# Kernel optimization log

Measured on AMD Instinct MI355X. Metric: run time of the kernel, lower is better.

The kernel has to match this reference:

```python
import jax, jax.numpy as jnp
import numpy as np

N = 100_000      # n_nodes
DEG = 32         # edge_threshold (fixed out-degree)
D = 64           # in_channels = out_channels, heads = 1
NEG_SLOPE = 0.2


def setup_inputs() -> dict:
    key = jax.random.key(0)
    k1, k2, k3, k4 = jax.random.split(key, 4)
    x = jax.random.normal(k1, (N, D), jnp.float32)
    # fixed-degree edge list with no self loops (offset in [1, N-1])
    src = jnp.repeat(jnp.arange(N, dtype=jnp.int64), DEG)
    off = jax.random.randint(k2, (N * DEG,), 1, N, dtype=jnp.int64)
    dst = (src + off) % N
    edge_index = jnp.stack([src, dst])  # [2, E]
    # glorot init as in the torch module
    stdv_w = float(np.sqrt(6.0 / (D + D)))
    weight = jax.random.uniform(k3, (D, D), jnp.float32, -stdv_w, stdv_w)
    stdv_a = float(np.sqrt(6.0 / (1 + 2 * D)))  # att is [1, heads=1, 2*D]
    att = jax.random.uniform(k4, (2 * D,), jnp.float32, -stdv_a, stdv_a)
    bias = jnp.zeros((D,), jnp.float32)
    return {"x": x, "edge_index": edge_index, "weight": weight, "att": att, "bias": bias}


def reference(x, edge_index, weight, att, bias):
    n, d = x.shape
    h = x @ weight                               # [N, D] (heads=1)
    # add self loops (inputs are constructed without self loops)
    loop = jnp.arange(n, dtype=edge_index.dtype)
    src = jnp.concatenate([edge_index[0], loop])  # message sources (x_j)
    dst = jnp.concatenate([edge_index[1], loop])  # aggregation targets (x_i)
    # GAT edge score: (cat([x_i, x_j]) * att).sum(-1) = h_i@a_i + h_j@a_j
    a_i, a_j = att[:d], att[d:]
    s_i = h @ a_i                                 # [N]
    s_j = h @ a_j                                 # [N]
    alpha = s_i[dst] + s_j[src]                   # [E+N]
    alpha = jnp.where(alpha > 0, alpha, NEG_SLOPE * alpha)  # leaky_relu
    # segment softmax over destination nodes (numerically stable)
    amax = jax.ops.segment_max(alpha, dst, num_segments=n)
    e = jnp.exp(alpha - amax[dst])
    denom = jax.ops.segment_sum(e, dst, num_segments=n)
    w = e / (denom[dst] + 1e-16)                  # [E+N]
    # weighted scatter-add aggregation of source features
    out = jax.ops.segment_sum(h[src] * w[:, None], dst, num_segments=n)  # [N, D]
    out = out + bias                              # head-mean is identity (heads=1)
    # dropout(p=0.5) is identity in eval mode; F.normalize (L2, dim=1, eps=1e-12)
    norm = jnp.linalg.norm(out, axis=1, keepdims=True)
    return out / jnp.maximum(norm, 1e-12)
```

## Files before the change

### kernel.cpp

```cpp
#include <hip/hip_runtime.h>
#include <math.h>

#define NEG_SLOPE 0.2f
#define NBINS_MAX 392
#define CURSOR_PAD 16
#define CHUNK_B 12500
#define CAPL 72
#define STRL 73
#define GRAN 16
#define CAP_SLOTS 12544
#define COLS_CAP 8704
#define CAPN 96
#define STRN 97
#define SENT 0xFFFFFFFFu

__device__ __forceinline__ unsigned pk_bf16x2(float a, float b) {
    unsigned ua = __float_as_uint(a);
    ua = (ua + 0x7FFFu + ((ua >> 16) & 1u)) >> 16;
    unsigned ub = __float_as_uint(b);
    ub = (ub + 0x7FFFu + ((ub >> 16) & 1u)) & 0xFFFF0000u;
    return ua | ub;
}

__global__ __launch_bounds__(256) void k_linear(const float* __restrict__ x,
        const float* __restrict__ W, const float* __restrict__ att,
        uint2* __restrict__ h16, float* __restrict__ si, float* __restrict__ sj,
        int* __restrict__ bin_cursor, int nbins, int n)
{
    int tid = threadIdx.x;
    int g = blockIdx.x * 256 + tid;
    if (g < nbins * CURSOR_PAD) bin_cursor[g] = 0;

    int lane = tid & 63;
    int wv = tid >> 6;
    int q = lane >> 4;
    int f = lane & 15;

    const float4* W4 = (const float4*)W;
    float4 Wr[16];
#pragma unroll
    for (int kb = 0; kb < 16; ++kb)
        Wr[kb] = W4[(16 * q + kb) * 16 + f];

    const float4* att4 = (const float4*)att;
    float4 ai4 = att4[f];
    float4 aj4 = att4[16 + f];
    const float4* x4 = (const float4*)x;

    int row0 = (blockIdx.x * 4 + wv) * 8;
    for (int r = 0; r < 8; ++r) {
        int row = row0 + r;
        if (row >= n) break;
        size_t xb = (size_t)row * 16 + 4 * q;
        float4 xq0 = x4[xb + 0];
        float4 xq1 = x4[xb + 1];
        float4 xq2 = x4[xb + 2];
        float4 xq3 = x4[xb + 3];
        float4 acc = {0.f, 0.f, 0.f, 0.f};
#define LSTEP(xc, kb) { float4 w4 = Wr[kb]; \
        acc.x = fmaf((xc), w4.x, acc.x); acc.y = fmaf((xc), w4.y, acc.y); \
        acc.z = fmaf((xc), w4.z, acc.z); acc.w = fmaf((xc), w4.w, acc.w); }
        LSTEP(xq0.x, 0)  LSTEP(xq0.y, 1)  LSTEP(xq0.z, 2)  LSTEP(xq0.w, 3)
        LSTEP(xq1.x, 4)  LSTEP(xq1.y, 5)  LSTEP(xq1.z, 6)  LSTEP(xq1.w, 7)
        LSTEP(xq2.x, 8)  LSTEP(xq2.y, 9)  LSTEP(xq2.z, 10) LSTEP(xq2.w, 11)
        LSTEP(xq3.x, 12) LSTEP(xq3.y, 13) LSTEP(xq3.z, 14) LSTEP(xq3.w, 15)
#undef LSTEP
        acc.x += __shfl_xor(acc.x, 16); acc.x += __shfl_xor(acc.x, 32);
        acc.y += __shfl_xor(acc.y, 16); acc.y += __shfl_xor(acc.y, 32);
        acc.z += __shfl_xor(acc.z, 16); acc.z += __shfl_xor(acc.z, 32);
        acc.w += __shfl_xor(acc.w, 16); acc.w += __shfl_xor(acc.w, 32);

        if (q == 0) {
            uint2 p;
            p.x = pk_bf16x2(acc.x, acc.y);
            p.y = pk_bf16x2(acc.z, acc.w);
            h16[(size_t)row * 16 + f] = p;
        }

        float p = acc.x * ai4.x + acc.y * ai4.y + acc.z * ai4.z + acc.w * ai4.w;
        float pq = acc.x * aj4.x + acc.y * aj4.y + acc.z * aj4.z + acc.w * aj4.w;
#pragma unroll
        for (int o = 8; o >= 1; o >>= 1) {
            p += __shfl_xor(p, o);
            pq += __shfl_xor(pq, o);
        }
        if (lane == 0) { si[row] = p; sj[row] = pq; }
    }
}

__global__ __launch_bounds__(512) void k_bin(const int* __restrict__ src,
        const int* __restrict__ dst, int E, int nbins,
        int* __restrict__ bin_cursor, unsigned* __restrict__ bin_edges)
{
    __shared__ unsigned bins[NBINS_MAX * STRL];
    __shared__ int cnt[NBINS_MAX];
    __shared__ int gbase[NBINS_MAX];

    int tid = threadIdx.x;
    int base = blockIdx.x * CHUNK_B;
    int cntE = E - base;
    if (cntE > CHUNK_B) cntE = CHUNK_B;
    int c4 = cntE >> 2;

    for (int b = tid; b < nbins; b += 512) cnt[b] = 0;
    __syncthreads();

#define PLACE(dd, ss) { int bb = (dd) >> 8; int c = atomicAdd(&cnt[bb], 1); \
        if (c < CAPL) bins[bb * STRL + c] = ((unsigned)((dd) & 255) << 17) | (unsigned)(ss); }
    {
        const int4* dst4 = (const int4*)(dst + base);
        const int4* src4 = (const int4*)(src + base);
        for (int i = tid; i < c4; i += 512) {
            int4 d4 = dst4[i];
            int4 s4 = src4[i];
            PLACE(d4.x, s4.x) PLACE(d4.y, s4.y) PLACE(d4.z, s4.z) PLACE(d4.w, s4.w)
        }
        for (int i = (c4 << 2) + tid; i < cntE; i += 512) {
            int dd = dst[base + i]; int ss = src[base + i];
            PLACE(dd, ss)
        }
    }
#undef PLACE
    __syncthreads();

    {
        int start = (blockIdx.x * 97) % nbins;
        for (int k = tid; k < nbins; k += 512) {
            int b = k + start;
            if (b >= nbins) b -= nbins;
            int c = cnt[b];
            if (c > CAPL) c = CAPL;
            int slots = (c + GRAN - 1) & ~(GRAN - 1);
            int g = (slots > 0) ? atomicAdd(&bin_cursor[b * CURSOR_PAD], slots) : 0;
            int allow = CAP_SLOTS - g;
            if (allow < 0) allow = 0;
            if (slots > allow) slots = allow;
            if (c > slots) c = slots;
            cnt[b] = c | (slots << 16);
            gbase[b] = b * CAP_SLOTS + g;
        }
    }
    __syncthreads();

    int lane = tid & 63;
    int wv = tid >> 6;
    for (int b = wv; b < nbins; b += 8) {
        int packed = cnt[b];
        int c = packed & 0xFFFF;
        int slots = packed >> 16;
        unsigned* dp = bin_edges + gbase[b];
        const unsigned* sp = bins + b * STRL;
        if (lane < slots)      dp[lane]      = (lane < c)      ? sp[lane]      : SENT;
        if (lane + 64 < slots) dp[lane + 64] = (lane + 64 < c) ? sp[lane + 64] : SENT;
    }
}

__global__ __launch_bounds__(512) void k_csr(const int* __restrict__ bin_cursor,
        const unsigned* __restrict__ bin_edges, unsigned* __restrict__ cols,
        int* __restrict__ row_start, int* __restrict__ deg, int n)
{
    __shared__ unsigned slots[256 * STRN];
    __shared__ int cntv[256];
    __shared__ int offv[256];
    __shared__ int wsum[4];
    int b = blockIdx.x;
    int tid = threadIdx.x;
    int base = b * CAP_SLOTS;
    int cbase = b * COLS_CAP;
    int cntE = bin_cursor[b * CURSOR_PAD];
    if (cntE > CAP_SLOTS) cntE = CAP_SLOTS;
    int c4 = cntE >> 2;

    if (tid < 256) cntv[tid] = 0;
    __syncthreads();

#define PUT(pkv) { unsigned pk = (pkv); if (pk != SENT) { int nl = (int)(pk >> 17); \
        int c = atomicAdd(&cntv[nl], 1); \
        if (c < CAPN) slots[nl * STRN + c] = pk & 0x1FFFFu; } }
    {
        const uint4* be4 = (const uint4*)(bin_edges + base);
        for (int i = tid; i < c4; i += 512) {
            uint4 p = be4[i];
            PUT(p.x) PUT(p.y) PUT(p.z) PUT(p.w)
        }
        for (int i = (c4 << 2) + tid; i < cntE; i += 512)
            PUT(bin_edges[base + i])
    }
#undef PUT
    __syncthreads();

    int lane = tid & 63;
    int wv = tid >> 6;
    int s = 0, v = 0;
    if (tid < 256) {
        s = cntv[tid];
        if (s > CAPN) s = CAPN;
        v = s;
#pragma unroll
        for (int o = 1; o < 64; o <<= 1) {
            int t = __shfl_up(v, o);
            if (lane >= o) v += t;
        }
        if (lane == 63) wsum[wv] = v;
    }
    __syncthreads();
    if (tid < 256) {
        int woff = 0;
        for (int w = 0; w < wv; ++w) woff += wsum[w];
        int ex = v - s + woff;
        int gd = b * 256 + tid;
        if (gd < n) {
            row_start[gd] = cbase + ex;
            deg[gd] = s;
        }
        offv[tid] = ex;
        cntv[tid] = s;
    }
    __syncthreads();

    for (int nl = wv; nl < 256; nl += 8) {
        int c = cntv[nl];
        int ex = offv[nl];
        if (lane < c)      cols[cbase + ex + lane]      = slots[nl * STRN + lane];
        if (lane + 64 < c) cols[cbase + ex + lane + 64] = slots[nl * STRN + lane + 64];
    }
}

__global__ __launch_bounds__(256) void k_agg(const uint2* __restrict__ h16,
        const float* __restrict__ si, const float* __restrict__ sj,
        const int* __restrict__ row_start, const int* __restrict__ deg_arr,
        const unsigned* __restrict__ cols,
        const float* __restrict__ bias, float* __restrict__ out, int n)
{
    __shared__ int2 swArr[4][132];
    int lane = threadIdx.x & 63;
    int wv = threadIdx.x >> 6;
    int d = blockIdx.x * 4 + wv;
    if (d >= n) return;

    int dg = deg_arr[d];
    if (dg > 128) dg = 128;
    int rs = row_start[d];
    float sid = si[d];

    int s0 = 0, s1 = 0;
    float a0 = -1e30f, a1 = -1e30f;
    if (lane < dg) {
        s0 = (int)cols[rs + lane];
        float t = sid + sj[s0];
        a0 = t > 0.f ? t : NEG_SLOPE * t;
    }
    if (lane + 64 < dg) {
        s1 = (int)cols[rs + lane + 64];
        float t = sid + sj[s1];
        a1 = t > 0.f ? t : NEG_SLOPE * t;
    }
    float tself = sid + sj[d];
    float aself = tself > 0.f ? tself : NEG_SLOPE * tself;

    float m = fmaxf(fmaxf(a0, a1), aself);
#pragma unroll
    for (int o = 32; o >= 1; o >>= 1) m = fmaxf(m, __shfl_xor(m, o));

    float e0 = (lane < dg) ? __expf(a0 - m) : 0.f;
    float e1 = (lane + 64 < dg) ? __expf(a1 - m) : 0.f;
    float eself = __expf(aself - m);

    float dsum = e0 + e1;
#pragma unroll
    for (int o = 32; o >= 1; o >>= 1) dsum += __shfl_xor(dsum, o);
    dsum += eself;

    if (lane < dg) swArr[wv][lane] = make_int2(s0, __float_as_int(e0));
    if (lane + 64 < dg) swArr[wv][lane + 64] = make_int2(s1, __float_as_int(e1));
    if (lane == 0) swArr[wv][dg] = make_int2(d, __float_as_int(eself));
    int cntAll = dg + 1;

    int q = lane >> 4;
    int f = lane & 15;
    int fb = f << 3;
    const char* h8 = (const char*)h16;
    float4 acc0 = {0.f, 0.f, 0.f, 0.f};
    float4 acc1 = {0.f, 0.f, 0.f, 0.f};
    float4 acc2 = {0.f, 0.f, 0.f, 0.f};
    float4 acc3 = {0.f, 0.f, 0.f, 0.f};

#define GLOAD(e) (*(const uint2*)(h8 + (((unsigned)(e) << 7) | fb)))
#define UNPK_FMA(hv, wgt, acc) { \
        acc.x = fmaf((wgt), __uint_as_float((hv).x << 16), acc.x); \
        acc.y = fmaf((wgt), __uint_as_float((hv).x & 0xFFFF0000u), acc.y); \
        acc.z = fmaf((wgt), __uint_as_float((hv).y << 16), acc.z); \
        acc.w = fmaf((wgt), __uint_as_float((hv).y & 0xFFFF0000u), acc.w); }

    int j = q;
    for (; j + 12 < cntAll; j += 16) {
        int2 eA = swArr[wv][j];
        int2 eB = swArr[wv][j + 4];
        int2 eC = swArr[wv][j + 8];
        int2 eD = swArr[wv][j + 12];
        uint2 hA = GLOAD(eA.x);
        uint2 hB = GLOAD(eB.x);
        uint2 hC = GLOAD(eC.x);
        uint2 hD = GLOAD(eD.x);
        float wA = __int_as_float(eA.y);
        float wB = __int_as_float(eB.y);
        float wC = __int_as_float(eC.y);
        float wD = __int_as_float(eD.y);
        UNPK_FMA(hA, wA, acc0)
        UNPK_FMA(hB, wB, acc1)
        UNPK_FMA(hC, wC, acc2)
        UNPK_FMA(hD, wD, acc3)
    }
    for (; j + 4 < cntAll; j += 8) {
        int2 eA = swArr[wv][j];
        int2 eB = swArr[wv][j + 4];
        uint2 hA = GLOAD(eA.x);
        uint2 hB = GLOAD(eB.x);
        float wA = __int_as_float(eA.y);
        float wB = __int_as_float(eB.y);
        UNPK_FMA(hA, wA, acc0)
        UNPK_FMA(hB, wB, acc1)
    }
    if (j < cntAll) {
        int2 eA = swArr[wv][j];
        uint2 hA = GLOAD(eA.x);
        float wA = __int_as_float(eA.y);
        UNPK_FMA(hA, wA, acc0)
    }
#undef UNPK_FMA
#undef GLOAD

    acc0.x += acc1.x; acc0.y += acc1.y; acc0.z += acc1.z; acc0.w += acc1.w;
    acc2.x += acc3.x; acc2.y += acc3.y; acc2.z += acc3.z; acc2.w += acc3.w;
    acc0.x += acc2.x; acc0.y += acc2.y; acc0.z += acc2.z; acc0.w += acc2.w;

    acc0.x += __shfl_xor(acc0.x, 16); acc0.x += __shfl_xor(acc0.x, 32);
    acc0.y += __shfl_xor(acc0.y, 16); acc0.y += __shfl_xor(acc0.y, 32);
    acc0.z += __shfl_xor(acc0.z, 16); acc0.z += __shfl_xor(acc0.z, 32);
    acc0.w += __shfl_xor(acc0.w, 16); acc0.w += __shfl_xor(acc0.w, 32);

    float inv = 1.f / (dsum + 1e-16f);
    const float4* b4 = (const float4*)bias;
    float4 bb = b4[f];
    float4 o4;
    o4.x = acc0.x * inv + bb.x;
    o4.y = acc0.y * inv + bb.y;
    o4.z = acc0.z * inv + bb.z;
    o4.w = acc0.w * inv + bb.w;

    float nsq = o4.x * o4.x + o4.y * o4.y + o4.z * o4.z + o4.w * o4.w;
#pragma unroll
    for (int o = 8; o >= 1; o >>= 1) nsq += __shfl_xor(nsq, o);
    float rn = 1.f / fmaxf(sqrtf(nsq), 1e-12f);

    if (q == 0) {
        float4 res;
        res.x = o4.x * rn; res.y = o4.y * rn; res.z = o4.z * rn; res.w = o4.w * rn;
        ((float4*)out)[(size_t)d * 16 + f] = res;
    }
}

extern "C" void kernel_launch(void* const* d_in, const int* in_sizes, int n_in,
                              void* d_out, int out_size, void* d_ws, size_t ws_size,
                              hipStream_t stream)
{
    const float* x    = (const float*)d_in[0];
    const int*   ei   = (const int*)d_in[1];
    const float* W    = (const float*)d_in[2];
    const float* att  = (const float*)d_in[3];
    const float* bias = (const float*)d_in[4];
    float* out = (float*)d_out;

    int n = in_sizes[0] / 64;
    int E = in_sizes[1] / 2;
    const int* src = ei;
    const int* dst = ei + E;

    int nbins = (n + 255) >> 8;
    int NCH = (E + CHUNK_B - 1) / CHUNK_B;

    char* ws = (char*)d_ws;
#define CARVE(ptr, type, count) type* ptr = (type*)ws; \
        ws += (((size_t)(count) * sizeof(type)) + 255) & ~(size_t)255;
    CARVE(h16, uint2, (size_t)n * 16)
    CARVE(si, float, n)
    CARVE(sj, float, n)
    CARVE(row_start, int, n)
    CARVE(deg, int, n)
    CARVE(bin_cursor, int, (size_t)NBINS_MAX * CURSOR_PAD)
    CARVE(bin_edges, unsigned, (size_t)nbins * CAP_SLOTS)
    CARVE(cols, unsigned, (size_t)nbins * COLS_CAP)
#undef CARVE

    k_linear<<<(n + 31) / 32, 256, 0, stream>>>(x, W, att, h16, si, sj, bin_cursor, nbins, n);
    k_bin<<<NCH, 512, 0, stream>>>(src, dst, E, nbins, bin_cursor, bin_edges);
    k_csr<<<nbins, 512, 0, stream>>>(bin_cursor, bin_edges, cols, row_start, deg, n);
    k_agg<<<(n + 3) / 4, 256, 0, stream>>>(h16, si, sj, row_start, deg, cols, bias, out, n);
}
```

Measured before the change: 238.9 us.

## Fuse CSR construction and attention aggregation into one per-bin kernel

Merges k_csr and k_agg into a single kernel. Each 256-node bin's neighbour lists stay in shared memory, and waves loop over that bin's destination nodes to run the softmax and weighted gather there. This removes the global cols/row_start/deg arrays, their write and re-read, and one kernel launch. The trade-off is far fewer blocks: one per bin, with a large shared-memory footprint, so less parallelism is available to hide gather latency. Per-node capacity also drops to 72 in-edges.

```diff
diff --git a/kernel.cpp b/kernel.cpp
--- a/kernel.cpp
+++ b/kernel.cpp
@@ -9,9 +9,8 @@
 #define STRL 73
 #define GRAN 16
 #define CAP_SLOTS 12544
-#define COLS_CAP 8704
-#define CAPN 96
-#define STRN 97
+#define CAPN 72
+#define STRN 73
 #define SENT 0xFFFFFFFFu
 
 __device__ __forceinline__ unsigned pk_bf16x2(float a, float b) {
@@ -155,18 +154,17 @@
     }
 }
 
-__global__ __launch_bounds__(512) void k_csr(const int* __restrict__ bin_cursor,
-        const unsigned* __restrict__ bin_edges, unsigned* __restrict__ cols,
-        int* __restrict__ row_start, int* __restrict__ deg, int n)
+__global__ __launch_bounds__(512) void k_fused(const int* __restrict__ bin_cursor,
+        const unsigned* __restrict__ bin_edges, const uint2* __restrict__ h16,
+        const float* __restrict__ si, const float* __restrict__ sj,
+        const float* __restrict__ bias, float* __restrict__ out, int n)
 {
     __shared__ unsigned slots[256 * STRN];
     __shared__ int cntv[256];
-    __shared__ int offv[256];
-    __shared__ int wsum[4];
+    __shared__ float ew[8][80];
     int b = blockIdx.x;
     int tid = threadIdx.x;
     int base = b * CAP_SLOTS;
-    int cbase = b * COLS_CAP;
     int cntE = bin_cursor[b * CURSOR_PAD];
     if (cntE > CAP_SLOTS) cntE = CAP_SLOTS;
     int c4 = cntE >> 2;
@@ -191,99 +189,58 @@
 
     int lane = tid & 63;
     int wv = tid >> 6;
-    int s = 0, v = 0;
-    if (tid < 256) {
-        s = cntv[tid];
-        if (s > CAPN) s = CAPN;
-        v = s;
-#pragma unroll
-        for (int o = 1; o < 64; o <<= 1) {
-            int t = __shfl_up(v, o);
-            if (lane >= o) v += t;
-        }
-        if (lane == 63) wsum[wv] = v;
-    }
-    __syncthreads();
-    if (tid < 256) {
-        int woff = 0;
-        for (int w = 0; w < wv; ++w) woff += wsum[w];
-        int ex = v - s + woff;
-        int gd = b * 256 + tid;
-        if (gd < n) {
-            row_start[gd] = cbase + ex;
-            deg[gd] = s;
-        }
-        offv[tid] = ex;
-        cntv[tid] = s;
-    }
-    __syncthreads();
-
-    for (int nl = wv; nl < 256; nl += 8) {
-        int c = cntv[nl];
-        int ex = offv[nl];
-        if (lane < c)      cols[cbase + ex + lane]      = slots[nl * STRN + lane];
-        if (lane + 64 < c) cols[cbase + ex + lane + 64] = slots[nl * STRN + lane + 64];
-    }
-}
-
-__global__ __launch_bounds__(256) void k_agg(const uint2* __restrict__ h16,
-        const float* __restrict__ si, const float* __restrict__ sj,
-        const int* __restrict__ row_start, const int* __restrict__ deg_arr,
-        const unsigned* __restrict__ cols,
-        const float* __restrict__ bias, float* __restrict__ out, int n)
-{
-    __shared__ int2 swArr[4][132];
-    int lane = threadIdx.x & 63;
-    int wv = threadIdx.x >> 6;
-    int d = blockIdx.x * 4 + wv;
-    if (d >= n) return;
-
-    int dg = deg_arr[d];
-    if (dg > 128) dg = 128;
-    int rs = row_start[d];
-    float sid = si[d];
-
-    int s0 = 0, s1 = 0;
-    float a0 = -1e30f, a1 = -1e30f;
-    if (lane < dg) {
-        s0 = (int)cols[rs + lane];
-        float t = sid + sj[s0];
-        a0 = t > 0.f ? t : NEG_SLOPE * t;
-    }
-    if (lane + 64 < dg) {
-        s1 = (int)cols[rs + lane + 64];
-        float t = sid + sj[s1];
-        a1 = t > 0.f ? t : NEG_SLOPE * t;
-    }
-    float tself = sid + sj[d];
-    float aself = tself > 0.f ? tself : NEG_SLOPE * tself;
-
-    float m = fmaxf(fmaxf(a0, a1), aself);
-#pragma unroll
-    for (int o = 32; o >= 1; o >>= 1) m = fmaxf(m, __shfl_xor(m, o));
-
-    float e0 = (lane < dg) ? __expf(a0 - m) : 0.f;
-    float e1 = (lane + 64 < dg) ? __expf(a1 - m) : 0.f;
-    float eself = __expf(aself - m);
-
-    float dsum = e0 + e1;
-#pragma unroll
-    for (int o = 32; o >= 1; o >>= 1) dsum += __shfl_xor(dsum, o);
-    dsum += eself;
-
-    if (lane < dg) swArr[wv][lane] = make_int2(s0, __float_as_int(e0));
-    if (lane + 64 < dg) swArr[wv][lane + 64] = make_int2(s1, __float_as_int(e1));
-    if (lane == 0) swArr[wv][dg] = make_int2(d, __float_as_int(eself));
-    int cntAll = dg + 1;
-
     int q = lane >> 4;
     int f = lane & 15;
     int fb = f << 3;
     const char* h8 = (const char*)h16;
-    float4 acc0 = {0.f, 0.f, 0.f, 0.f};
-    float4 acc1 = {0.f, 0.f, 0.f, 0.f};
-    float4 acc2 = {0.f, 0.f, 0.f, 0.f};
-    float4 acc3 = {0.f, 0.f, 0.f, 0.f};
+    const float4* b4p = (const float4*)bias;
+    float4 bb = b4p[f];
+
+    for (int nl = wv; nl < 256; nl += 8) {
+        int d = b * 256 + nl;
+        if (d >= n) break;
+        int dg = cntv[nl];
+        if (dg > CAPN) dg = CAPN;
+        float sid = si[d];
+        unsigned* scol = slots + nl * STRN;
+
+        int s0 = 0, s1 = 0;
+        float a0 = -1e30f, a1 = -1e30f;
+        if (lane < dg) {
+            s0 = (int)scol[lane];
+            float t = sid + sj[s0];
+            a0 = t > 0.f ? t : NEG_SLOPE * t;
+        }
+        if (lane + 64 < dg) {
+            s1 = (int)scol[lane + 64];
+            float t = sid + sj[s1];
+            a1 = t > 0.f ? t : NEG_SLOPE * t;
+        }
+        float tself = sid + sj[d];
+        float aself = tself > 0.f ? tself : NEG_SLOPE * tself;
+
+        float m = fmaxf(fmaxf(a0, a1), aself);
+#pragma unroll
+        for (int o = 32; o >= 1; o >>= 1) m = fmaxf(m, __shfl_xor(m, o));
+
+        float e0 = (lane < dg) ? __expf(a0 - m) : 0.f;
+        float e1 = (lane + 64 < dg) ? __expf(a1 - m) : 0.f;
+        float eself = __expf(aself - m);
+
+        float dsum = e0 + e1;
+#pragma unroll
+        for (int o = 32; o >= 1; o >>= 1) dsum += __shfl_xor(dsum, o);
+        dsum += eself;
+
+        if (lane < dg) ew[wv][lane] = e0;
+        if (lane + 64 < dg) ew[wv][lane + 64] = e1;
+        if (lane == 0) { scol[dg] = (unsigned)d; ew[wv][dg] = eself; }
+        int cntAll = dg + 1;
+
+        float4 acc0 = {0.f, 0.f, 0.f, 0.f};
+        float4 acc1 = {0.f, 0.f, 0.f, 0.f};
+        float4 acc2 = {0.f, 0.f, 0.f, 0.f};
+        float4 acc3 = {0.f, 0.f, 0.f, 0.f};
 
 #define GLOAD(e) (*(const uint2*)(h8 + (((unsigned)(e) << 7) | fb)))
 #define UNPK_FMA(hv, wgt, acc) { \
@@ -292,71 +249,63 @@
         acc.z = fmaf((wgt), __uint_as_float((hv).y << 16), acc.z); \
         acc.w = fmaf((wgt), __uint_as_float((hv).y & 0xFFFF0000u), acc.w); }
 
-    int j = q;
-    for (; j + 12 < cntAll; j += 16) {
-        int2 eA = swArr[wv][j];
-        int2 eB = swArr[wv][j + 4];
-        int2 eC = swArr[wv][j + 8];
-        int2 eD = swArr[wv][j + 12];
-        uint2 hA = GLOAD(eA.x);
-        uint2 hB = GLOAD(eB.x);
-        uint2 hC = GLOAD(eC.x);
-        uint2 hD = GLOAD(eD.x);
-        float wA = __int_as_float(eA.y);
-        float wB = __int_as_float(eB.y);
-        float wC = __int_as_float(eC.y);
-        float wD = __int_as_float(eD.y);
-        UNPK_FMA(hA, wA, acc0)
-        UNPK_FMA(hB, wB, acc1)
-        UNPK_FMA(hC, wC, acc2)
-        UNPK_FMA(hD, wD, acc3)
-    }
-    for (; j + 4 < cntAll; j += 8) {
-        int2 eA = swArr[wv][j];
-        int2 eB = swArr[wv][j + 4];
-        uint2 hA = GLOAD(eA.x);
-        uint2 hB = GLOAD(eB.x);
-        float wA = __int_as_float(eA.y);
-        float wB = __int_as_float(eB.y);
-        UNPK_FMA(hA, wA, acc0)
-        UNPK_FMA(hB, wB, acc1)
-    }
-    if (j < cntAll) {
-        int2 eA = swArr[wv][j];
-        uint2 hA = GLOAD(eA.x);
-        float wA = __int_as_float(eA.y);
-        UNPK_FMA(hA, wA, acc0)
-    }
+        int j = q;
+        for (; j + 12 < cntAll; j += 16) {
+            unsigned sA = scol[j];      float wA = ew[wv][j];
+            unsigned sB = scol[j + 4];  float wB = ew[wv][j + 4];
+            unsigned sC = scol[j + 8];  float wC = ew[wv][j + 8];
+            unsigned sD = scol[j + 12]; float wD = ew[wv][j + 12];
+            uint2 hA = GLOAD(sA);
+            uint2 hB = GLOAD(sB);
+            uint2 hC = GLOAD(sC);
+            uint2 hD = GLOAD(sD);
+            UNPK_FMA(hA, wA, acc0)
+            UNPK_FMA(hB, wB, acc1)
+            UNPK_FMA(hC, wC, acc2)
+            UNPK_FMA(hD, wD, acc3)
+        }
+        for (; j + 4 < cntAll; j += 8) {
+            unsigned sA = scol[j];     float wA = ew[wv][j];
+            unsigned sB = scol[j + 4]; float wB = ew[wv][j + 4];
+            uint2 hA = GLOAD(sA);
+            uint2 hB = GLOAD(sB);
+            UNPK_FMA(hA, wA, acc0)
+            UNPK_FMA(hB, wB, acc1)
+        }
+        if (j < cntAll) {
+            unsigned sA = scol[j]; float wA = ew[wv][j];
+            uint2 hA = GLOAD(sA);
+            UNPK_FMA(hA, wA, acc0)
+        }
 #undef UNPK_FMA
 #undef GLOAD
 
-    acc0.x += acc1.x; acc0.y += acc1.y; acc0.z += acc1.z; acc0.w += acc1.w;
-    acc2.x += acc3.x; acc2.y += acc3.y; acc2.z += acc3.z; acc2.w += acc3.w;
-    acc0.x += acc2.x; acc0.y += acc2.y; acc0.z += acc2.z; acc0.w += acc2.w;
-
-    acc0.x += __shfl_xor(acc0.x, 16); acc0.x += __shfl_xor(acc0.x, 32);
-    acc0.y += __shfl_xor(acc0.y, 16); acc0.y += __shfl_xor(acc0.y, 32);
-    acc0.z += __shfl_xor(acc0.z, 16); acc0.z += __shfl_xor(acc0.z, 32);
-    acc0.w += __shfl_xor(acc0.w, 16); acc0.w += __shfl_xor(acc0.w, 32);
-
-    float inv = 1.f / (dsum + 1e-16f);
-    const float4* b4 = (const float4*)bias;
-    float4 bb = b4[f];
-    float4 o4;
-    o4.x = acc0.x * inv + bb.x;
-    o4.y = acc0.y * inv + bb.y;
-    o4.z = acc0.z * inv + bb.z;
-    o4.w = acc0.w * inv + bb.w;
-
-    float nsq = o4.x * o4.x + o4.y * o4.y + o4.z * o4.z + o4.w * o4.w;
-#pragma unroll
-    for (int o = 8; o >= 1; o >>= 1) nsq += __shfl_xor(nsq, o);
-    float rn = 1.f / fmaxf(sqrtf(nsq), 1e-12f);
-
-    if (q == 0) {
-        float4 res;
-        res.x = o4.x * rn; res.y = o4.y * rn; res.z = o4.z * rn; res.w = o4.w * rn;
-        ((float4*)out)[(size_t)d * 16 + f] = res;
+        acc0.x += acc1.x; acc0.y += acc1.y; acc0.z += acc1.z; acc0.w += acc1.w;
+        acc2.x += acc3.x; acc2.y += acc3.y; acc2.z += acc3.z; acc2.w += acc3.w;
+        acc0.x += acc2.x; acc0.y += acc2.y; acc0.z += acc2.z; acc0.w += acc2.w;
+
+        acc0.x += __shfl_xor(acc0.x, 16); acc0.x += __shfl_xor(acc0.x, 32);
+        acc0.y += __shfl_xor(acc0.y, 16); acc0.y += __shfl_xor(acc0.y, 32);
+        acc0.z += __shfl_xor(acc0.z, 16); acc0.z += __shfl_xor(acc0.z, 32);
+        acc0.w += __shfl_xor(acc0.w, 16); acc0.w += __shfl_xor(acc0.w, 32);
+
+        float inv = 1.f / (dsum + 1e-16f);
+        float4 o4;
+        o4.x = acc0.x * inv + bb.x;
+        o4.y = acc0.y * inv + bb.y;
+        o4.z = acc0.z * inv + bb.z;
+        o4.w = acc0.w * inv + bb.w;
+
+        float nsq = o4.x * o4.x + o4.y * o4.y + o4.z * o4.z + o4.w * o4.w;
+#pragma unroll
+        for (int o = 8; o >= 1; o >>= 1) nsq += __shfl_xor(nsq, o);
+        float rn = 1.f / fmaxf(sqrtf(nsq), 1e-12f);
+
+        if (q == 0) {
+            float4 res;
+            res.x = o4.x * rn; res.y = o4.y * rn; res.z = o4.z * rn; res.w = o4.w * rn;
+            ((float4*)out)[(size_t)d * 16 + f] = res;
+        }
     }
 }
 
@@ -385,15 +334,11 @@
     CARVE(h16, uint2, (size_t)n * 16)
     CARVE(si, float, n)
     CARVE(sj, float, n)
-    CARVE(row_start, int, n)
-    CARVE(deg, int, n)
     CARVE(bin_cursor, int, (size_t)NBINS_MAX * CURSOR_PAD)
     CARVE(bin_edges, unsigned, (size_t)nbins * CAP_SLOTS)
-    CARVE(cols, unsigned, (size_t)nbins * COLS_CAP)
 #undef CARVE
 
     k_linear<<<(n + 31) / 32, 256, 0, stream>>>(x, W, att, h16, si, sj, bin_cursor, nbins, n);
     k_bin<<<NCH, 512, 0, stream>>>(src, dst, E, nbins, bin_cursor, bin_edges);
-    k_csr<<<nbins, 512, 0, stream>>>(bin_cursor, bin_edges, cols, row_start, deg, n);
-    k_agg<<<(n + 3) / 4, 256, 0, stream>>>(h16, si, sj, row_start, deg, cols, bias, out, n);
-}
+    k_fused<<<nbins, 512, 0, stream>>>(bin_cursor, bin_edges, h16, si, sj, bias, out, n);
+}
```

After: 259.2 us. 8.5% more time.
